# Kernel optimization log

Measured on AMD Instinct MI355X. Metric: run time of the kernel, lower is better.

## Reference

```python
import jax, jax.numpy as jnp
import numpy as np

EMBED_DIM = 512
NUM_HEADS = 8
HEAD_DIM = EMBED_DIM // NUM_HEADS
SCALE = HEAD_DIM ** -0.5


def setup_inputs() -> dict:
    key = jax.random.key(0)
    ks = jax.random.split(key, 12)
    B, Nq, Nk, C = 2, 2048, 2048, EMBED_DIM
    # xavier_uniform bound for square CxC weights
    bound = float(np.sqrt(6.0 / (C + C)))
    def w(k):
        return jax.random.uniform(k, (C, C), jnp.float32, -bound, bound)
    return {
        "query": jax.random.normal(ks[0], (B, Nq, C), jnp.float32),
        "key": jax.random.normal(ks[1], (B, Nk, C), jnp.float32),
        "value": jax.random.normal(ks[2], (B, Nk, C), jnp.float32),
        "key_padding_mask": jnp.zeros((B, Nk), dtype=bool),
        "Wq": w(ks[3]), "bq": jnp.zeros((C,), jnp.float32),
        "Wk": w(ks[4]), "bk": jnp.zeros((C,), jnp.float32),
        "Wv": w(ks[5]), "bv": jnp.zeros((C,), jnp.float32),
        "Wo": w(ks[6]), "bo": jnp.zeros((C,), jnp.float32),
    }


def reference(query, key, value, key_padding_mask, Wq, bq, Wk, bk, Wv, bv, Wo, bo):
    B, Nq, C = query.shape
    Nk = key.shape[1]
    H, D = NUM_HEADS, HEAD_DIM
    # torch Linear: x @ W.T + b
    Q = (query @ Wq.T + bq).reshape(B, Nq, H, D).transpose(0, 2, 1, 3)  # (B,H,Nq,D)
    K = (key @ Wk.T + bk).reshape(B, Nk, H, D).transpose(0, 2, 1, 3)
    V = (value @ Wv.T + bv).reshape(B, Nk, H, D).transpose(0, 2, 1, 3)
    scores = jnp.einsum("bhqd,bhkd->bhqk", Q, K) * SCALE  # (B,H,Nq,Nk)
    scores = jnp.where(key_padding_mask[:, None, None, :], -jnp.inf, scores)
    attn = jax.nn.softmax(scores, axis=-1)
    out = jnp.einsum("bhqk,bhkd->bhqd", attn, V)  # (B,H,Nq,D)
    out = out.transpose(0, 2, 1, 3).reshape(B, Nq, C)
    return out @ Wo.T + bo
```

## Files before the change

kernel.cpp:

```cpp
#include <hip/hip_runtime.h>

typedef unsigned short u16;
typedef __attribute__((ext_vector_type(8))) short short8;
typedef __attribute__((ext_vector_type(8))) __bf16 bf16x8;
typedef __attribute__((ext_vector_type(4))) float f32x4;
typedef __attribute__((ext_vector_type(4))) unsigned int u32x4;

#define MFMA_BF16(a, b, c) __builtin_amdgcn_mfma_f32_16x16x32_bf16((a), (b), (c), 0, 0, 0)

__device__ __forceinline__ u16 f2bf(float f) {
    unsigned u = __builtin_bit_cast(unsigned, f);
    u += 0x7FFFu + ((u >> 16) & 1u);
    return (u16)(u >> 16);
}

__device__ __forceinline__ float bf2f(short s) {
    unsigned u = ((unsigned)(u16)s) << 16;
    return __builtin_bit_cast(float, u);
}

__device__ __forceinline__ unsigned cvt_pk_bf16(float lo, float hi) {
    unsigned r;
    asm("v_cvt_pk_bf16_f32 %0, %1, %2" : "=v"(r) : "v"(lo), "v"(hi));
    return r;
}

__device__ __forceinline__ float fast_exp2(float x) {
    float r;
    asm("v_exp_f32 %0, %1" : "=v"(r) : "v"(x));
    return r;
}

__global__ __launch_bounds__(256) void proj_gemm(
    const float* __restrict__ Xq, const float* __restrict__ Xk, const float* __restrict__ Xv,
    const float* __restrict__ Wq, const float* __restrict__ Wk, const float* __restrict__ Wv,
    const float* __restrict__ bq, const float* __restrict__ bk, const float* __restrict__ bv,
    u16* __restrict__ Oq, u16* __restrict__ Ok, u16* __restrict__ Ov)
{
    constexpr int K = 512, N = 512;
    const int z = blockIdx.z;
    const float* __restrict__ X = (z == 0) ? Xq : (z == 1) ? Xk : Xv;
    const float* __restrict__ W = (z == 0) ? Wq : (z == 1) ? Wk : Wv;
    const float* __restrict__ bias = (z == 0) ? bq : (z == 1) ? bk : bv;
    u16* __restrict__ O = (z == 0) ? Oq : (z == 1) ? Ok : Ov;
    const float alpha = (z == 0) ? 0.125f * 1.44269504088896f : 1.0f;

    __shared__ u16 lA[128 * 64];
    __shared__ u16 lB[128 * 64];

    const int tid = threadIdx.x, lane = tid & 63, w = tid >> 6;
    const int wr = w >> 1, wc = w & 1;
    const int bm = blockIdx.x, bn = blockIdx.y;
    const int r0 = tid >> 3, cc = tid & 7;

    f32x4 acc[4][4];
    for (int m = 0; m < 4; ++m)
        for (int n = 0; n < 4; ++n)
            acc[m][n] = f32x4{0.f, 0.f, 0.f, 0.f};

    for (int kt = 0; kt < K; kt += 64) {
        __syncthreads();
        for (int p = 0; p < 4; ++p) {
            int r = r0 + p * 32;
            {
                const float4* g = (const float4*)(X + (size_t)(bm * 128 + r) * K + kt + cc * 8);
                float4 f0 = g[0], f1 = g[1];
                short8 v;
                v[0] = (short)f2bf(f0.x); v[1] = (short)f2bf(f0.y);
                v[2] = (short)f2bf(f0.z); v[3] = (short)f2bf(f0.w);
                v[4] = (short)f2bf(f1.x); v[5] = (short)f2bf(f1.y);
                v[6] = (short)f2bf(f1.z); v[7] = (short)f2bf(f1.w);
                *(short8*)&lA[r * 64 + ((cc ^ (r & 7)) << 3)] = v;
            }
            {
                const float4* g = (const float4*)(W + (size_t)(bn * 128 + r) * K + kt + cc * 8);
                float4 f0 = g[0], f1 = g[1];
                short8 v;
                v[0] = (short)f2bf(f0.x); v[1] = (short)f2bf(f0.y);
                v[2] = (short)f2bf(f0.z); v[3] = (short)f2bf(f0.w);
                v[4] = (short)f2bf(f1.x); v[5] = (short)f2bf(f1.y);
                v[6] = (short)f2bf(f1.z); v[7] = (short)f2bf(f1.w);
                *(short8*)&lB[r * 64 + ((cc ^ (r & 7)) << 3)] = v;
            }
        }
        __syncthreads();
        for (int kk = 0; kk < 2; ++kk) {
            bf16x8 af[4], bfr[4];
            for (int m = 0; m < 4; ++m) {
                int row = wr * 64 + m * 16 + (lane & 15);
                af[m] = *(const bf16x8*)&lA[row * 64 + (((kk * 4 + (lane >> 4)) ^ (row & 7)) << 3)];
            }
            for (int n = 0; n < 4; ++n) {
                int row = wc * 64 + n * 16 + (lane & 15);
                bfr[n] = *(const bf16x8*)&lB[row * 64 + (((kk * 4 + (lane >> 4)) ^ (row & 7)) << 3)];
            }
            for (int m = 0; m < 4; ++m)
                for (int n = 0; n < 4; ++n)
                    acc[m][n] = MFMA_BF16(af[m], bfr[n], acc[m][n]);
        }
    }
    for (int m = 0; m < 4; ++m)
        for (int n = 0; n < 4; ++n) {
            int row = bm * 128 + wr * 64 + m * 16 + ((lane >> 4) << 2);
            int col = bn * 128 + wc * 64 + n * 16 + (lane & 15);
            float bv_ = bias[col];
            for (int i = 0; i < 4; ++i) {
                float v = (acc[m][n][i] + bv_) * alpha;
                O[(size_t)(row + i) * N + col] = f2bf(v);
            }
        }
}

__global__ __launch_bounds__(256) void merge_k(
    const u16* __restrict__ Op0, const u16* __restrict__ Op1,
    const float2* __restrict__ ml0, const float2* __restrict__ ml1,
    u16* __restrict__ Ob)
{
    int idx = blockIdx.x * 256 + threadIdx.x;
    int row = idx >> 6;
    int c8 = idx & 63;
    int h = c8 >> 3;
    int b = row >> 11;
    int mli = (b * 8 + h) * 2048 + (row & 2047);
    float2 v0 = ml0[mli], v1 = ml1[mli];
    float m = fmaxf(v0.x, v1.x);
    float e0 = exp2f(v0.x - m) * v0.y;
    float e1 = exp2f(v1.x - m) * v1.y;
    float inv = 1.f / (e0 + e1);
    float w0 = e0 * inv, w1 = e1 * inv;
    size_t off = (size_t)row * 512 + c8 * 8;
    short8 a0 = *(const short8*)(Op0 + off);
    short8 a1 = *(const short8*)(Op1 + off);
    short8 v;
    #pragma unroll
    for (int j = 0; j < 8; ++j)
        v[j] = (short)f2bf(bf2f(a0[j]) * w0 + bf2f(a1[j]) * w1);
    *(short8*)(Ob + off) = v;
}

__global__ __launch_bounds__(256) void out_gemm(
    const u16* __restrict__ A, const float* __restrict__ W,
    const float* __restrict__ bias, float* __restrict__ O)
{
    constexpr int K = 512, N = 512;
    __shared__ u16 lA[128 * 64];
    __shared__ u16 lB[128 * 64];

    const int tid = threadIdx.x, lane = tid & 63, w = tid >> 6;
    const int wr = w >> 1, wc = w & 1;
    const int bm = blockIdx.x, bn = blockIdx.y;
    const int r0 = tid >> 3, cc = tid & 7;

    f32x4 acc[4][4];
    for (int m = 0; m < 4; ++m)
        for (int n = 0; n < 4; ++n)
            acc[m][n] = f32x4{0.f, 0.f, 0.f, 0.f};

    for (int kt = 0; kt < K; kt += 64) {
        __syncthreads();
        for (int p = 0; p < 4; ++p) {
            int r = r0 + p * 32;
            *(short8*)&lA[r * 64 + ((cc ^ (r & 7)) << 3)] =
                *(const short8*)(A + (size_t)(bm * 128 + r) * K + kt + cc * 8);
            const float4* g = (const float4*)(W + (size_t)(bn * 128 + r) * K + kt + cc * 8);
            float4 f0 = g[0], f1 = g[1];
            short8 v;
            v[0] = (short)f2bf(f0.x); v[1] = (short)f2bf(f0.y);
            v[2] = (short)f2bf(f0.z); v[3] = (short)f2bf(f0.w);
            v[4] = (short)f2bf(f1.x); v[5] = (short)f2bf(f1.y);
            v[6] = (short)f2bf(f1.z); v[7] = (short)f2bf(f1.w);
            *(short8*)&lB[r * 64 + ((cc ^ (r & 7)) << 3)] = v;
        }
        __syncthreads();
        for (int kk = 0; kk < 2; ++kk) {
            bf16x8 af[4], bfr[4];
            for (int m = 0; m < 4; ++m) {
                int row = wr * 64 + m * 16 + (lane & 15);
                af[m] = *(const bf16x8*)&lA[row * 64 + (((kk * 4 + (lane >> 4)) ^ (row & 7)) << 3)];
            }
            for (int n = 0; n < 4; ++n) {
                int row = wc * 64 + n * 16 + (lane & 15);
                bfr[n] = *(const bf16x8*)&lB[row * 64 + (((kk * 4 + (lane >> 4)) ^ (row & 7)) << 3)];
            }
            for (int m = 0; m < 4; ++m)
                for (int n = 0; n < 4; ++n)
                    acc[m][n] = MFMA_BF16(af[m], bfr[n], acc[m][n]);
        }
    }
    for (int m = 0; m < 4; ++m)
        for (int n = 0; n < 4; ++n) {
            int row = bm * 128 + wr * 64 + m * 16 + ((lane >> 4) << 2);
            int col = bn * 128 + wc * 64 + n * 16 + (lane & 15);
            float bv_ = bias[col];
            for (int i = 0; i < 4; ++i)
                O[(size_t)(row + i) * N + col] = acc[m][n][i] + bv_;
        }
}

__global__ __launch_bounds__(256, 4) void attn_k(
    const u16* __restrict__ Qp, const u16* __restrict__ Kp, const u16* __restrict__ Vp,
    const unsigned char* __restrict__ mask,
    u16* __restrict__ Op0, u16* __restrict__ Op1,
    float2* __restrict__ ml0, float2* __restrict__ ml1)
{
    constexpr int C = 512, NK = 2048, KVH = 1024, NT = KVH / 64;
    __shared__ u16 lK[64 * 64];
    __shared__ u16 lV[64 * 64];

    const int tid = threadIdx.x, lane = tid & 63, w = tid >> 6;
    const int gd = lane >> 4, q15 = lane & 15;
    const int bh = blockIdx.x, qb = blockIdx.y, z = blockIdx.z;
    const int b = bh >> 3, h = bh & 7;
    const size_t qrow0 = (size_t)b * 2048 + qb * 64;
    const size_t krow0 = (size_t)b * 2048 + (size_t)z * KVH;
    const int col0 = h * 64;
    const int rs = tid >> 3, cc = tid & 7;

    u16* __restrict__ Op = z ? Op1 : Op0;
    float2* __restrict__ ml = z ? ml1 : ml0;

    bf16x8 qf[2];
    {
        const u16* qrow = Qp + (qrow0 + w * 16 + q15) * C + col0;
        qf[0] = *(const bf16x8*)(qrow + gd * 8);
        qf[1] = *(const bf16x8*)(qrow + 32 + gd * 8);
    }

    float mst = -1e30f, lstp = 0.f;
    f32x4 oacc[4];
    #pragma unroll
    for (int i = 0; i < 4; ++i) oacc[i] = f32x4{0.f, 0.f, 0.f, 0.f};

    short8 kpre[2], vpre[2];
    #pragma unroll
    for (int p = 0; p < 2; ++p) {
        kpre[p] = *(const short8*)(Kp + (krow0 + rs + p * 32) * C + col0 + cc * 8);
        vpre[p] = *(const short8*)(Vp + (krow0 + rs + p * 32) * C + col0 + cc * 8);
    }

    for (int t = 0; t < NT; ++t) {
        __syncthreads();
        #pragma unroll
        for (int p = 0; p < 2; ++p) {
            int r = rs + p * 32;
            *(short8*)&lK[r * 64 + ((cc ^ (r & 7)) << 3)] = kpre[p];
            #pragma unroll
            for (int j = 0; j < 8; ++j)
                lV[(cc * 8 + j) * 64 + (((r >> 3) ^ ((j + cc) & 7)) << 3) + (r & 7)] = (u16)vpre[p][j];
        }
        if (t + 1 < NT) {
            #pragma unroll
            for (int p = 0; p < 2; ++p) {
                kpre[p] = *(const short8*)(Kp + (krow0 + (t + 1) * 64 + rs + p * 32) * C + col0 + cc * 8);
                vpre[p] = *(const short8*)(Vp + (krow0 + (t + 1) * 64 + rs + p * 32) * C + col0 + cc * 8);
            }
        }
        __syncthreads();

        unsigned char mby = mask[(size_t)b * NK + z * KVH + t * 64 + lane];

        f32x4 s[4];
        #pragma unroll
        for (int i = 0; i < 4; ++i) s[i] = f32x4{0.f, 0.f, 0.f, 0.f};
        __builtin_amdgcn_s_setprio(1);
        #pragma unroll
        for (int kb = 0; kb < 2; ++kb)
            #pragma unroll
            for (int t4 = 0; t4 < 4; ++t4) {
                int krow = t4 * 16 + q15;
                bf16x8 kf = *(const bf16x8*)&lK[krow * 64 + (((kb * 4 + gd) ^ (krow & 7)) << 3)];
                s[t4] = MFMA_BF16(kf, qf[kb], s[t4]);
            }
        __builtin_amdgcn_s_setprio(0);

        unsigned long long m64 = __ballot(mby != 0);
        if (m64) {
            #pragma unroll
            for (int t4 = 0; t4 < 4; ++t4)
                #pragma unroll
                for (int i = 0; i < 4; ++i) {
                    int k = t4 * 16 + gd * 4 + i;
                    if ((m64 >> k) & 1ull) s[t4][i] = -1e30f;
                }
        }

        float pmax = s[0][0];
        #pragma unroll
        for (int t4 = 0; t4 < 4; ++t4)
            #pragma unroll
            for (int i = 0; i < 4; ++i) pmax = fmaxf(pmax, s[t4][i]);

        if (!__all(pmax - mst <= 11.0f)) {
            float rm = fmaxf(pmax, __shfl_xor(pmax, 16));
            rm = fmaxf(rm, __shfl_xor(rm, 32));
            float mn = fmaxf(mst, rm);
            float sf = exp2f(mst - mn);
            mst = mn;
            lstp *= sf;
            #pragma unroll
            for (int i = 0; i < 4; ++i) {
                float sfi = __shfl(sf, (lane & 48) | ((gd << 2) + i));
                #pragma unroll
                for (int t2 = 0; t2 < 4; ++t2) oacc[t2][i] *= sfi;
            }
        }

        float rsum = 0.f;
        #pragma unroll
        for (int t4 = 0; t4 < 4; ++t4)
            #pragma unroll
            for (int i = 0; i < 4; ++i) {
                float e = fast_exp2(s[t4][i] - mst);
                s[t4][i] = e;
                rsum += e;
            }
        lstp += rsum;

        __builtin_amdgcn_s_setprio(1);
        #pragma unroll
        for (int kb = 0; kb < 2; ++kb) {
            u32x4 pw;
            pw[0] = cvt_pk_bf16(s[2 * kb][0], s[2 * kb][1]);
            pw[1] = cvt_pk_bf16(s[2 * kb][2], s[2 * kb][3]);
            pw[2] = cvt_pk_bf16(s[2 * kb + 1][0], s[2 * kb + 1][1]);
            pw[3] = cvt_pk_bf16(s[2 * kb + 1][2], s[2 * kb + 1][3]);
            bf16x8 pa = __builtin_bit_cast(bf16x8, pw);
            #pragma unroll
            for (int t2 = 0; t2 < 4; ++t2) {
                int d = t2 * 16 + q15;
                int swd = (d + (d >> 3)) & 7;
                int base = d * 64 + 4 * (gd & 1);
                uint2 v0 = *(const uint2*)&lV[base + (((4 * kb + 0 + (gd >> 1)) ^ swd) << 3)];
                uint2 v1 = *(const uint2*)&lV[base + (((4 * kb + 2 + (gd >> 1)) ^ swd) << 3)];
                u32x4 vw; vw[0] = v0.x; vw[1] = v0.y; vw[2] = v1.x; vw[3] = v1.y;
                bf16x8 vf = __builtin_bit_cast(bf16x8, vw);
                oacc[t2] = MFMA_BF16(pa, vf, oacc[t2]);
            }
        }
        __builtin_amdgcn_s_setprio(0);
    }

    float lsum = lstp + __shfl_xor(lstp, 16);
    lsum += __shfl_xor(lsum, 32);

    if (gd == 0)
        ml[bh * 2048 + qb * 64 + w * 16 + q15] = make_float2(mst, lsum);

    #pragma unroll
    for (int i = 0; i < 4; ++i) {
        float li = __shfl(lsum, (lane & 48) | ((gd << 2) + i));
        float inv = 1.f / li;
        int qg = qb * 64 + w * 16 + gd * 4 + i;
        #pragma unroll
        for (int t2 = 0; t2 < 4; ++t2) {
            int col = col0 + t2 * 16 + q15;
            Op[((size_t)b * 2048 + qg) * C + col] = f2bf(oacc[t2][i] * inv);
        }
    }
}

extern "C" void kernel_launch(void* const* d_in, const int* in_sizes, int n_in,
                              void* d_out, int out_size, void* d_ws, size_t ws_size,
                              hipStream_t stream) {
    const float* query = (const float*)d_in[0];
    const float* key   = (const float*)d_in[1];
    const float* value = (const float*)d_in[2];
    const unsigned char* mask = (const unsigned char*)d_in[3];
    const float* Wq = (const float*)d_in[4];
    const float* bq = (const float*)d_in[5];
    const float* Wk = (const float*)d_in[6];
    const float* bk = (const float*)d_in[7];
    const float* Wv = (const float*)d_in[8];
    const float* bv = (const float*)d_in[9];
    const float* Wo = (const float*)d_in[10];
    const float* bo = (const float*)d_in[11];

    u16* ws = (u16*)d_ws;
    u16* Qp  = ws;
    u16* Kp  = ws + 2097152;
    u16* Vp  = ws + 4194304;
    u16* Op0 = ws + 6291456;
    u16* Op1 = ws + 8388608;
    float2* ml0 = (float2*)(ws + 10485760);
    float2* ml1 = (float2*)(ws + 10485760 + 131072);
    u16* Ob = Qp;

    dim3 gp(32, 4, 3);
    proj_gemm<<<gp, 256, 0, stream>>>(query, key, value, Wq, Wk, Wv, bq, bk, bv, Qp, Kp, Vp);

    dim3 ga(16, 32, 2);
    attn_k<<<ga, 256, 0, stream>>>(Qp, Kp, Vp, mask, Op0, Op1, ml0, ml1);

    merge_k<<<1024, 256, 0, stream>>>(Op0, Op1, ml0, ml1, Ob);

    dim3 go(32, 4);
    out_gemm<<<go, 256, 0, stream>>>(Ob, Wo, bo, (float*)d_out);
}
```

Baseline: 77.13 us.

## Double-buffer K/V in LDS with direct global-to-LDS K loads in attention

The attention kernel now keeps two LDS buffers for K and V. K tiles are fetched straight into LDS with global_load_lds, V is prefetched two tiles ahead through registers, and the mask bytes are preloaded into packed registers. Each iteration uses one barrier with explicit waitcnts instead of two __syncthreads, so loads for the next tile overlap compute on the current one. This doubles LDS use, which may limit occupancy, and the hand-written vmcnt counts must match the number of outstanding loads or results will be wrong.

Result: slower. 82.98 us (+7.6%).

```diff
diff --git a/kernel.cpp b/kernel.cpp
--- a/kernel.cpp
+++ b/kernel.cpp
@@ -29,6 +29,12 @@
     float r;
     asm("v_exp_f32 %0, %1" : "=v"(r) : "v"(x));
     return r;
+}
+
+__device__ __forceinline__ void gload16(const u16* g, u16* l) {
+    __builtin_amdgcn_global_load_lds(
+        (const __attribute__((address_space(1))) void*)g,
+        (__attribute__((address_space(3))) void*)l, 16, 0, 0);
 }
 
 __global__ __launch_bounds__(256) void proj_gemm(
@@ -204,8 +210,8 @@
     float2* __restrict__ ml0, float2* __restrict__ ml1)
 {
     constexpr int C = 512, NK = 2048, KVH = 1024, NT = KVH / 64;
-    __shared__ u16 lK[64 * 64];
-    __shared__ u16 lV[64 * 64];
+    __shared__ u16 lK[2][64 * 64];
+    __shared__ u16 lV[2][64 * 64];
 
     const int tid = threadIdx.x, lane = tid & 63, w = tid >> 6;
     const int gd = lane >> 4, q15 = lane & 15;
@@ -219,6 +225,10 @@
     u16* __restrict__ Op = z ? Op1 : Op0;
     float2* __restrict__ ml = z ? ml1 : ml0;
 
+    const int klrow = w * 8 + (lane >> 3);
+    const int ksw = (lane & 7) ^ (klrow & 7);
+    const u16* kbase = Kp + (krow0 + klrow) * C + col0 + (ksw << 3);
+
     bf16x8 qf[2];
     {
         const u16* qrow = Qp + (qrow0 + w * 16 + q15) * C + col0;
@@ -226,38 +236,69 @@
         qf[1] = *(const bf16x8*)(qrow + 32 + gd * 8);
     }
 
+    unsigned long long mpk0 = 0ull, mpk1 = 0ull;
+    {
+        const unsigned char* mrow = mask + (size_t)b * NK + z * KVH + lane;
+        #pragma unroll
+        for (int tt = 0; tt < 8; ++tt) {
+            mpk0 |= (unsigned long long)mrow[tt * 64] << (8 * tt);
+            mpk1 |= (unsigned long long)mrow[(tt + 8) * 64] << (8 * tt);
+        }
+    }
+
     float mst = -1e30f, lstp = 0.f;
     f32x4 oacc[4];
     #pragma unroll
     for (int i = 0; i < 4; ++i) oacc[i] = f32x4{0.f, 0.f, 0.f, 0.f};
 
-    short8 kpre[2], vpre[2];
+    gload16(kbase, &lK[0][(w * 8) * 64]);
+    gload16(kbase + 32 * C, &lK[0][(32 + w * 8) * 64]);
+    short8 vpre[2];
+    #pragma unroll
+    for (int p = 0; p < 2; ++p)
+        vpre[p] = *(const short8*)(Vp + (krow0 + rs + p * 32) * C + col0 + cc * 8);
     #pragma unroll
     for (int p = 0; p < 2; ++p) {
-        kpre[p] = *(const short8*)(Kp + (krow0 + rs + p * 32) * C + col0 + cc * 8);
-        vpre[p] = *(const short8*)(Vp + (krow0 + rs + p * 32) * C + col0 + cc * 8);
-    }
+        int r = rs + p * 32;
+        #pragma unroll
+        for (int j = 0; j < 8; ++j)
+            lV[0][(cc * 8 + j) * 64 + (((r >> 3) ^ ((j + cc) & 7)) << 3) + (r & 7)] = (u16)vpre[p][j];
+    }
+    #pragma unroll
+    for (int p = 0; p < 2; ++p)
+        vpre[p] = *(const short8*)(Vp + (krow0 + 64 + rs + p * 32) * C + col0 + cc * 8);
+    asm volatile("s_waitcnt lgkmcnt(0)" ::: "memory");
+    asm volatile("s_waitcnt vmcnt(0)" ::: "memory");
+    __builtin_amdgcn_s_barrier();
+    __builtin_amdgcn_sched_barrier(0);
 
     for (int t = 0; t < NT; ++t) {
-        __syncthreads();
-        #pragma unroll
-        for (int p = 0; p < 2; ++p) {
-            int r = rs + p * 32;
-            *(short8*)&lK[r * 64 + ((cc ^ (r & 7)) << 3)] = kpre[p];
-            #pragma unroll
-            for (int j = 0; j < 8; ++j)
-                lV[(cc * 8 + j) * 64 + (((r >> 3) ^ ((j + cc) & 7)) << 3) + (r & 7)] = (u16)vpre[p][j];
-        }
+        const int cur = t & 1, nxt = cur ^ 1;
+
         if (t + 1 < NT) {
+            const u16* ks = kbase + (size_t)(t + 1) * 64 * C;
+            gload16(ks, &lK[nxt][(w * 8) * 64]);
+            gload16(ks + 32 * C, &lK[nxt][(32 + w * 8) * 64]);
+        }
+        __builtin_amdgcn_sched_barrier(0);
+
+        if (t + 1 < NT) {
             #pragma unroll
             for (int p = 0; p < 2; ++p) {
-                kpre[p] = *(const short8*)(Kp + (krow0 + (t + 1) * 64 + rs + p * 32) * C + col0 + cc * 8);
-                vpre[p] = *(const short8*)(Vp + (krow0 + (t + 1) * 64 + rs + p * 32) * C + col0 + cc * 8);
-            }
-        }
-        __syncthreads();
-
-        unsigned char mby = mask[(size_t)b * NK + z * KVH + t * 64 + lane];
+                int r = rs + p * 32;
+                #pragma unroll
+                for (int j = 0; j < 8; ++j)
+                    lV[nxt][(cc * 8 + j) * 64 + (((r >> 3) ^ ((j + cc) & 7)) << 3) + (r & 7)] = (u16)vpre[p][j];
+            }
+        }
+        if (t + 2 < NT) {
+            #pragma unroll
+            for (int p = 0; p < 2; ++p)
+                vpre[p] = *(const short8*)(Vp + (krow0 + (size_t)(t + 2) * 64 + rs + p * 32) * C + col0 + cc * 8);
+        }
+
+        unsigned long long mm = (t & 8) ? mpk1 : mpk0;
+        unsigned char mby = (unsigned char)(mm >> ((t & 7) * 8));
 
         f32x4 s[4];
         #pragma unroll
@@ -268,7 +309,7 @@
             #pragma unroll
             for (int t4 = 0; t4 < 4; ++t4) {
                 int krow = t4 * 16 + q15;
-                bf16x8 kf = *(const bf16x8*)&lK[krow * 64 + (((kb * 4 + gd) ^ (krow & 7)) << 3)];
+                bf16x8 kf = *(const bf16x8*)&lK[cur][krow * 64 + (((kb * 4 + gd) ^ (krow & 7)) << 3)];
                 s[t4] = MFMA_BF16(kf, qf[kb], s[t4]);
             }
         __builtin_amdgcn_s_setprio(0);
@@ -330,14 +371,25 @@
                 int d = t2 * 16 + q15;
                 int swd = (d + (d >> 3)) & 7;
                 int base = d * 64 + 4 * (gd & 1);
-                uint2 v0 = *(const uint2*)&lV[base + (((4 * kb + 0 + (gd >> 1)) ^ swd) << 3)];
-                uint2 v1 = *(const uint2*)&lV[base + (((4 * kb + 2 + (gd >> 1)) ^ swd) << 3)];
+                uint2 v0 = *(const uint2*)&lV[cur][base + (((4 * kb + 0 + (gd >> 1)) ^ swd) << 3)];
+                uint2 v1 = *(const uint2*)&lV[cur][base + (((4 * kb + 2 + (gd >> 1)) ^ swd) << 3)];
                 u32x4 vw; vw[0] = v0.x; vw[1] = v0.y; vw[2] = v1.x; vw[3] = v1.y;
                 bf16x8 vf = __builtin_bit_cast(bf16x8, vw);
                 oacc[t2] = MFMA_BF16(pa, vf, oacc[t2]);
             }
         }
         __builtin_amdgcn_s_setprio(0);
+
+        if (t + 1 < NT) {
+            asm volatile("s_waitcnt lgkmcnt(0)" ::: "memory");
+            if (t + 2 < NT) {
+                asm volatile("s_waitcnt vmcnt(2)" ::: "memory");
+            } else {
+                asm volatile("s_waitcnt vmcnt(0)" ::: "memory");
+            }
+            __builtin_amdgcn_s_barrier();
+            __builtin_amdgcn_sched_barrier(0);
+        }
     }
 
     float lsum = lstp + __shfl_xor(lstp, 16);
```
